# Optimization experiments

Measured on AMD Instinct MI355X. Metric: run time of the kernel, lower is better.

Reference implementation:

```python
import jax, jax.numpy as jnp
import numpy as np

L, B, S, D, H, F = 4, 2, 2048, 768, 12, 3072
HD = D // H
EPS = 1e-5


def _ln(x, g, b):
    m = jnp.mean(x, axis=-1, keepdims=True)
    v = jnp.mean((x - m) ** 2, axis=-1, keepdims=True)
    return (x - m) * jax.lax.rsqrt(v + EPS) * g + b


def setup_inputs() -> dict:
    key = jax.random.key(0)
    ks = jax.random.split(key, 12)
    s = 0.02
    n = lambda k, shp: jax.random.normal(k, shp, jnp.float32) * s
    return {
        "inputs": jax.random.normal(ks[0], (B, S, D), jnp.float32),
        "attn_mask": jax.random.randint(ks[1], (B, S, S), 0, 2) == 1,
        "Wq": n(ks[2], (L, D, D)), "bq": jnp.zeros((L, D), jnp.float32),
        "Wk": n(ks[3], (L, D, D)), "bk": jnp.zeros((L, D), jnp.float32),
        "Wv": n(ks[4], (L, D, D)), "bv": jnp.zeros((L, D), jnp.float32),
        "Wo": n(ks[5], (L, D, D)), "bo": jnp.zeros((L, D), jnp.float32),
        "ln1_g": jnp.ones((L, D), jnp.float32), "ln1_b": jnp.zeros((L, D), jnp.float32),
        "W1": n(ks[6], (L, F, D)), "b1": jnp.zeros((L, F), jnp.float32),
        "W2": n(ks[7], (L, D, F)), "b2": jnp.zeros((L, D), jnp.float32),
        "ln2_g": jnp.ones((L, D), jnp.float32), "ln2_b": jnp.zeros((L, D), jnp.float32),
    }


def reference(inputs, attn_mask, Wq, bq, Wk, bk, Wv, bv, Wo, bo,
              ln1_g, ln1_b, W1, b1, W2, b2, ln2_g, ln2_b):
    x = inputs
    scale = 1.0 / (HD ** 0.5)
    mask = attn_mask[:, None, :, :]  # [B,1,S,S] broadcasts over heads
    nlayers = Wq.shape[0]
    for i in range(nlayers):
        # torch Linear: y = x @ W.T + b, W stored [out,in]
        q = (jnp.einsum('bsd,ed->bse', x, Wq[i]) + bq[i]).reshape(B, S, H, HD)
        k = (jnp.einsum('bsd,ed->bse', x, Wk[i]) + bk[i]).reshape(B, S, H, HD)
        v = (jnp.einsum('bsd,ed->bse', x, Wv[i]) + bv[i]).reshape(B, S, H, HD)
        scores = jnp.einsum('bqhd,bkhd->bhqk', q, k) * scale
        scores = jnp.where(mask, jnp.float32(-1e9), scores)
        p = jax.nn.softmax(scores, axis=-1)
        ctx = jnp.einsum('bhqk,bkhd->bqhd', p, v).reshape(B, S, D)
        attn = jnp.einsum('bsd,ed->bse', ctx, Wo[i]) + bo[i]
        x = _ln(attn + x, ln1_g[i], ln1_b[i])
        h = jax.nn.relu(jnp.einsum('bsd,fd->bsf', x, W1[i]) + b1[i])
        ff = jnp.einsum('bsf,df->bsd', h, W2[i]) + b2[i]
        x = _ln(ff + x, ln2_g[i], ln2_b[i])
    return x
```

## Files before the change

kernel.cpp:

```cpp
#include <hip/hip_runtime.h>
#include <cmath>
#include <cstdint>
#include <cstddef>


typedef __bf16 bf16_t;
typedef __bf16 bf16x8 __attribute__((ext_vector_type(8)));
typedef __bf16 bf16x4 __attribute__((ext_vector_type(4)));
typedef float  f32x4  __attribute__((ext_vector_type(4)));
typedef float  f32x16 __attribute__((ext_vector_type(16)));
typedef int    i32x2  __attribute__((ext_vector_type(2)));

#define DEV static __device__ __forceinline__

constexpr int Lc = 4, Bc = 2, Sc = 2048, Dc = 768, Hc = 12, Fc = 3072, HDc = 64;
constexpr int Mrows = Bc * Sc;
#define QSCALE 0.18033688011112042f

DEV f32x4 mfma16(bf16x8 a, bf16x8 b, f32x4 c) {
  return __builtin_amdgcn_mfma_f32_16x16x32_bf16(a, b, c, 0, 0, 0);
}
DEV f32x16 mfma32(bf16x8 a, bf16x8 b, f32x16 c) {
  return __builtin_amdgcn_mfma_f32_32x32x16_bf16(a, b, c, 0, 0, 0);
}

DEV void gload_lds16(const void* g, void* l) {
  __builtin_amdgcn_global_load_lds(
      (const __attribute__((address_space(1))) void*)g,
      (__attribute__((address_space(3))) void*)l,
      16, 0, 0);
}

DEV float fexp2(float x) { return __builtin_amdgcn_exp2f(x); }

DEV unsigned cvtpk(float lo, float hi_) {
  unsigned r;
  asm("v_cvt_pk_bf16_f32 %0, %1, %2" : "=v"(r) : "v"(lo), "v"(hi_));
  return r;
}
DEV void swapl(unsigned &a, unsigned &b) {
  i32x2 r = __builtin_amdgcn_permlane32_swap((int)a, (int)b, false, false);
  a = (unsigned)r[0];
  b = (unsigned)r[1];
}
DEV bf16x8 frag4(unsigned a, unsigned b, unsigned c, unsigned d) {
  union { unsigned u[4]; bf16x8 v; } x;
  x.u[0] = a; x.u[1] = b; x.u[2] = c; x.u[3] = d;
  return x.v;
}


__global__ __launch_bounds__(256) void cvt_bf16_kernel(const float* __restrict__ in,
                                                       bf16_t* __restrict__ out, int n) {
  int i = (blockIdx.x * 256 + threadIdx.x) * 4;
  if (i + 3 < n) {
    float4 v = *(const float4*)(in + i);
    bf16x4 o;
    o[0] = (bf16_t)v.x; o[1] = (bf16_t)v.y; o[2] = (bf16_t)v.z; o[3] = (bf16_t)v.w;
    *(bf16x4*)(out + i) = o;
  }
}

__global__ __launch_bounds__(256) void cvt_qkv_kernel(const float* __restrict__ in,
                                                      bf16_t* __restrict__ out,
                                                      int which, int n) {
  int i = (blockIdx.x * 256 + threadIdx.x) * 4;
  if (i + 3 < n) {
    int l = i / (Dc * Dc);
    float4 v = *(const float4*)(in + i);
    bf16x4 o;
    o[0] = (bf16_t)v.x; o[1] = (bf16_t)v.y; o[2] = (bf16_t)v.z; o[3] = (bf16_t)v.w;
    *(bf16x4*)(out + (size_t)i + (size_t)(2 * l + which) * Dc * Dc) = o;
  }
}

__global__ __launch_bounds__(256) void init_x_kernel(const float* __restrict__ in,
                                                     float* __restrict__ x,
                                                     bf16_t* __restrict__ xb, int n) {
  int i = (blockIdx.x * 256 + threadIdx.x) * 4;
  if (i + 3 < n) {
    float4 v = *(const float4*)(in + i);
    *(float4*)(x + i) = v;
    bf16x4 o;
    o[0] = (bf16_t)v.x; o[1] = (bf16_t)v.y; o[2] = (bf16_t)v.z; o[3] = (bf16_t)v.w;
    *(bf16x4*)(xb + i) = o;
  }
}

__global__ __launch_bounds__(256) void mask_packT_kernel(const int* __restrict__ m,
                                                         unsigned long long* __restrict__ bits) {
  size_t gid = (size_t)blockIdx.x * 256 + threadIdx.x;
  int l = (int)(gid & 63);
  size_t widx = gid >> 6;
  size_t q = widx & (Sc - 1);
  size_t bkw = widx >> 11;
  size_t kw = bkw & (Sc / 64 - 1);
  size_t b = bkw >> 5;
  unsigned long long bm = __ballot(m[(b * Sc + q) * Sc + kw * 64 + l] != 0);
  if (l == 0) bits[widx] = bm;
}

template <int MF, int EPI>
__global__ __launch_bounds__(256) void gemm_bt(const bf16_t* __restrict__ A,
                                               const bf16_t* __restrict__ Bm,
                                               const float* __restrict__ bias,
                                               float* __restrict__ Cf,
                                               bf16_t* __restrict__ Cb,
                                               int M, int N, int K) {
  constexpr int BM = MF * 32;
  __shared__ bf16_t sA[BM * 64];
  __shared__ bf16_t sB[128 * 64];
  const int tid = threadIdx.x;
  const int w = tid >> 6, l = tid & 63, lg = l >> 4, li = l & 15;
  const int wr = w >> 1, wc = w & 1;
  const int tm = blockIdx.x * BM, tn = blockIdx.y * 128;

  f32x4 acc[MF][4];
#pragma unroll
  for (int m = 0; m < MF; m++)
#pragma unroll
    for (int n = 0; n < 4; n++) acc[m][n] = (f32x4){0.f, 0.f, 0.f, 0.f};

  for (int k0 = 0; k0 < K; k0 += 64) {
#pragma unroll
    for (int i = 0; i < MF; i++) {
      int off = i * 2048 + tid * 8;
      gload_lds16(A + (size_t)(tm + (off >> 6)) * K + k0 + (off & 63),
                  &sA[i * 2048 + w * 512]);
    }
#pragma unroll
    for (int i = 0; i < 4; i++) {
      int off = i * 2048 + tid * 8;
      gload_lds16(Bm + (size_t)(tn + (off >> 6)) * K + k0 + (off & 63),
                  &sB[i * 2048 + w * 512]);
    }
    __syncthreads();
#pragma unroll
    for (int kk = 0; kk < 2; kk++) {
      bf16x8 af[MF], bfr[4];
#pragma unroll
      for (int m = 0; m < MF; m++)
        af[m] = *(const bf16x8*)&sA[(wr * MF * 16 + m * 16 + li) * 64 + kk * 32 + lg * 8];
#pragma unroll
      for (int n = 0; n < 4; n++)
        bfr[n] = *(const bf16x8*)&sB[(wc * 64 + n * 16 + li) * 64 + kk * 32 + lg * 8];
#pragma unroll
      for (int m = 0; m < MF; m++)
#pragma unroll
        for (int n = 0; n < 4; n++)
          acc[m][n] = mfma16(af[m], bfr[n], acc[m][n]);
    }
    __syncthreads();
  }

#pragma unroll
  for (int m = 0; m < MF; m++) {
    int rbase = tm + wr * MF * 16 + m * 16 + lg * 4;
#pragma unroll
    for (int n = 0; n < 4; n++) {
      int c = tn + wc * 64 + n * 16 + li;
      float bv = bias[c];
#pragma unroll
      for (int j = 0; j < 4; j++) {
        float v = acc[m][n][j] + bv;
        size_t idx = (size_t)(rbase + j) * N + c;
        if constexpr (EPI == 0) Cf[idx] = v;
        else Cb[idx] = (bf16_t)fmaxf(v, 0.f);
      }
    }
  }
}

__global__ __launch_bounds__(256) void gemm_qkv(const bf16_t* __restrict__ A,
                                                const bf16_t* __restrict__ Bm,
                                                const float* __restrict__ bq,
                                                const float* __restrict__ bk,
                                                const float* __restrict__ bv,
                                                bf16_t* __restrict__ qo,
                                                bf16_t* __restrict__ ko,
                                                bf16_t* __restrict__ vTo) {
  constexpr int K = Dc;
  __shared__ bf16_t sA[64 * 64];
  __shared__ bf16_t sB[128 * 64];
  const int tid = threadIdx.x;
  const int w = tid >> 6, l = tid & 63, lg = l >> 4, li = l & 15;
  const int wr = w >> 1, wc = w & 1;
  const int tm = blockIdx.x * 64, tn = blockIdx.y * 128;

  f32x4 acc[2][4];
#pragma unroll
  for (int m = 0; m < 2; m++)
#pragma unroll
    for (int n = 0; n < 4; n++) acc[m][n] = (f32x4){0.f, 0.f, 0.f, 0.f};

  for (int k0 = 0; k0 < K; k0 += 64) {
#pragma unroll
    for (int i = 0; i < 2; i++) {
      int off = i * 2048 + tid * 8;
      gload_lds16(A + (size_t)(tm + (off >> 6)) * K + k0 + (off & 63),
                  &sA[i * 2048 + w * 512]);
    }
#pragma unroll
    for (int i = 0; i < 4; i++) {
      int off = i * 2048 + tid * 8;
      gload_lds16(Bm + (size_t)(tn + (off >> 6)) * K + k0 + (off & 63),
                  &sB[i * 2048 + w * 512]);
    }
    __syncthreads();
#pragma unroll
    for (int kk = 0; kk < 2; kk++) {
      bf16x8 af[2], bfr[4];
#pragma unroll
      for (int m = 0; m < 2; m++)
        af[m] = *(const bf16x8*)&sA[(wr * 32 + m * 16 + li) * 64 + kk * 32 + lg * 8];
#pragma unroll
      for (int n = 0; n < 4; n++)
        bfr[n] = *(const bf16x8*)&sB[(wc * 64 + n * 16 + li) * 64 + kk * 32 + lg * 8];
#pragma unroll
      for (int m = 0; m < 2; m++)
#pragma unroll
        for (int n = 0; n < 4; n++)
          acc[m][n] = mfma16(af[m], bfr[n], acc[m][n]);
    }
    __syncthreads();
  }

  const int which = tn / 768;
#pragma unroll
  for (int m = 0; m < 2; m++) {
    int rbase = tm + wr * 32 + m * 16 + lg * 4;
#pragma unroll
    for (int n = 0; n < 4; n++) {
      int c = tn + wc * 64 + n * 16 + li;
      int col = c - which * 768;
      if (which == 0) {
        float bvv = bq[col];
#pragma unroll
        for (int j = 0; j < 4; j++)
          qo[(size_t)(rbase + j) * Dc + col] = (bf16_t)((acc[m][n][j] + bvv) * QSCALE);
      } else if (which == 1) {
        float bvv = bk[col];
#pragma unroll
        for (int j = 0; j < 4; j++)
          ko[(size_t)(rbase + j) * Dc + col] = (bf16_t)(acc[m][n][j] + bvv);
      } else {
        float bvv = bv[col];
        int h = col >> 6, d = col & 63;
        int b = rbase >> 11, s0 = rbase & 2047;
        bf16x4 pk;
#pragma unroll
        for (int j = 0; j < 4; j++) pk[j] = (bf16_t)(acc[m][n][j] + bvv);
        *(bf16x4*)(vTo + ((size_t)(b * Hc + h) * HDc + d) * Sc + s0) = pk;
      }
    }
  }
}

__global__ __launch_bounds__(128) void attn3_kernel(
    const bf16_t* __restrict__ q, const bf16_t* __restrict__ k,
    const bf16_t* __restrict__ vT, const unsigned long long* __restrict__ maskT,
    bf16_t* __restrict__ ctx) {
  __shared__ __align__(16) char smem[32768];

  const int t = threadIdx.x, w = t >> 6, l = t & 63;
  const int hi = l >> 5, li = l & 31, lx = li & 7;
  const int gid = blockIdx.x;
  const int rest = gid >> 3;
  const int qt = rest & 31, bh = (gid & 7) + 8 * (rest >> 5);
  const int b = bh / Hc, h = bh - b * Hc;
  const int qbase = qt * 64;
  const int qrow = qbase + w * 32 + li;

  const bf16_t* qp = q + (size_t)(b * Sc + qrow) * Dc + h * HDc + hi * 8;
  bf16x8 qf[4];
#pragma unroll
  for (int dk = 0; dk < 4; dk++) qf[dk] = *(const bf16x8*)(qp + dk * 16);

  const bf16_t* kg = k + (size_t)(b * Sc) * Dc + h * HDc;
  const bf16_t* vg = vT + (size_t)bh * HDc * Sc;
  const unsigned long long* mg = maskT + (size_t)b * (Sc / 64) * Sc + qrow;

  f32x16 o0, o1;
#pragma unroll
  for (int r = 0; r < 16; r++) { o0[r] = 0.f; o1[r] = 0.f; }
  float ps = 0.f;

  auto stage = [&](int buf, int c) {
    const int kv0 = c * 64;
    bf16_t* sk = (bf16_t*)(smem + buf * 8192);
    bf16_t* sv = (bf16_t*)(smem + 16384 + buf * 8192);
#pragma unroll
    for (int i = 0; i < 4; i++) {
      int s = i * 128 + t;
      int row = s >> 3, ch = s & 7;
      gload_lds16(kg + (size_t)(kv0 + row) * Dc + ((ch ^ (row & 7)) * 8),
                  sk + (i * 128 + w * 64) * 8);
    }
#pragma unroll
    for (int i = 0; i < 4; i++) {
      int s = i * 128 + t;
      int row = s >> 3, ch = s & 7;
      gload_lds16(vg + (size_t)row * Sc + kv0 + ((ch ^ (row & 7)) * 8),
                  sv + (i * 128 + w * 64) * 8);
    }
  };

  stage(0, 0);
  __syncthreads();
  int cur = 0;
  constexpr int NT = Sc / 64;
  for (int c = 0; c < NT; c++) {
    if (c + 1 < NT) stage(cur ^ 1, c + 1);
    unsigned long long mw = mg[(size_t)c * Sc];
    unsigned ms0 = ((unsigned)mw) >> (hi * 4);
    unsigned ms1 = ((unsigned)(mw >> 32)) >> (hi * 4);

    f32x16 sc0, sc1;
#pragma unroll
    for (int r = 0; r < 16; r++) { sc0[r] = 0.f; sc1[r] = 0.f; }
    const bf16_t* kb = (const bf16_t*)(smem + cur * 8192);
#pragma unroll
    for (int dk = 0; dk < 4; dk++) {
      int ch = dk * 2 + hi;
      bf16x8 ka0 = *(const bf16x8*)(kb + li * 64 + ((ch ^ lx) * 8));
      bf16x8 ka1 = *(const bf16x8*)(kb + (32 + li) * 64 + ((ch ^ lx) * 8));
      sc0 = mfma32(ka0, qf[dk], sc0);
      sc1 = mfma32(ka1, qf[dk], sc1);
    }

    unsigned pw[16];
#pragma unroll
    for (int r = 0; r < 16; r += 2) {
      int kbit = (r & 3) + 8 * (r >> 2);
      float a0 = fexp2(sc0[r]), a1 = fexp2(sc0[r + 1]);
      float b0 = fexp2(sc1[r]), b1 = fexp2(sc1[r + 1]);
      a0 = ((ms0 >> kbit) & 1u) ? 0.f : a0;
      a1 = ((ms0 >> (kbit + 1)) & 1u) ? 0.f : a1;
      b0 = ((ms1 >> kbit) & 1u) ? 0.f : b0;
      b1 = ((ms1 >> (kbit + 1)) & 1u) ? 0.f : b1;
      ps += (a0 + a1) + (b0 + b1);
      pw[r >> 1] = cvtpk(a0, a1);
      pw[8 + (r >> 1)] = cvtpk(b0, b1);
    }
    swapl(pw[0], pw[2]);  swapl(pw[1], pw[3]);
    swapl(pw[4], pw[6]);  swapl(pw[5], pw[7]);
    swapl(pw[8], pw[10]); swapl(pw[9], pw[11]);
    swapl(pw[12], pw[14]); swapl(pw[13], pw[15]);
    bf16x8 pb0 = frag4(pw[0], pw[1], pw[2], pw[3]);
    bf16x8 pb1 = frag4(pw[4], pw[5], pw[6], pw[7]);
    bf16x8 pb2 = frag4(pw[8], pw[9], pw[10], pw[11]);
    bf16x8 pb3 = frag4(pw[12], pw[13], pw[14], pw[15]);

    const bf16_t* vb = (const bf16_t*)(smem + 16384 + cur * 8192);
#pragma unroll
    for (int g = 0; g < 4; g++) {
      int ch = g * 2 + hi;
      bf16x8 va0 = *(const bf16x8*)(vb + li * 64 + ((ch ^ lx) * 8));
      bf16x8 va1 = *(const bf16x8*)(vb + (32 + li) * 64 + ((ch ^ lx) * 8));
      bf16x8 pbg = (g == 0) ? pb0 : (g == 1) ? pb1 : (g == 2) ? pb2 : pb3;
      o0 = mfma32(va0, pbg, o0);
      o1 = mfma32(va1, pbg, o1);
    }
    __syncthreads();
    cur ^= 1;
  }

  float tot = ps + __shfl_xor(ps, 32, 64);
  float inv = 1.f / tot;

  __syncthreads();
  char* so = smem + w * 4096;
#pragma unroll
  for (int g = 0; g < 4; g++) {
    unsigned u0 = cvtpk(o0[g * 4 + 0] * inv, o0[g * 4 + 1] * inv);
    unsigned u1 = cvtpk(o0[g * 4 + 2] * inv, o0[g * 4 + 3] * inv);
    unsigned v0 = cvtpk(o1[g * 4 + 0] * inv, o1[g * 4 + 1] * inv);
    unsigned v1 = cvtpk(o1[g * 4 + 2] * inv, o1[g * 4 + 3] * inv);
    *(uint2*)(so + li * 128 + ((g ^ lx) * 16) + hi * 8) = make_uint2(u0, u1);
    *(uint2*)(so + li * 128 + (((g + 4) ^ lx) * 16) + hi * 8) = make_uint2(v0, v1);
  }
  __syncthreads();
  bf16_t* cbase = ctx + (size_t)(b * Sc + qbase + w * 32) * Dc + h * HDc;
#pragma unroll
  for (int i = 0; i < 4; i++) {
    int s = i * 64 + l;
    int row = s >> 3, ch = s & 7;
    bf16x8 vv = *(const bf16x8*)(so + row * 128 + ((ch ^ (row & 7)) * 16));
    *(bf16x8*)(cbase + (size_t)row * Dc + ch * 8) = vv;
  }
}

__global__ __launch_bounds__(256) void ln_res_kernel(const float* __restrict__ a,
                                                     const float* r,
                                                     const float* __restrict__ g,
                                                     const float* __restrict__ bb,
                                                     float* xo, bf16_t* __restrict__ xb) {
  const int row = blockIdx.x;
  const int t = threadIdx.x;
  const float* pa = a + (size_t)row * Dc;
  const float* pr = r + (size_t)row * Dc;
  float v0 = pa[t] + pr[t];
  float v1 = pa[t + 256] + pr[t + 256];
  float v2 = pa[t + 512] + pr[t + 512];
  float s = v0 + v1 + v2;
  float sq = v0 * v0 + v1 * v1 + v2 * v2;
#pragma unroll
  for (int ofs = 1; ofs < 64; ofs <<= 1) {
    s += __shfl_xor(s, ofs, 64);
    sq += __shfl_xor(sq, ofs, 64);
  }
  __shared__ float red[8];
  const int w = t >> 6, l = t & 63;
  if (l == 0) { red[w] = s; red[4 + w] = sq; }
  __syncthreads();
  s = red[0] + red[1] + red[2] + red[3];
  sq = red[4] + red[5] + red[6] + red[7];
  const float mean = s * (1.f / Dc);
  const float var = sq * (1.f / Dc) - mean * mean;
  const float rs = rsqrtf(var + 1e-5f);
  float* po = xo + (size_t)row * Dc;
  bf16_t* pb = xb + (size_t)row * Dc;
#pragma unroll
  for (int i = 0; i < 3; i++) {
    int d = t + i * 256;
    float vv = (i == 0 ? v0 : (i == 1 ? v1 : v2));
    float ov = (vv - mean) * rs * g[d] + bb[d];
    po[d] = ov;
    pb[d] = (bf16_t)ov;
  }
}


extern "C" void kernel_launch(void* const* d_in, const int* in_sizes, int n_in,
                              void* d_out, int out_size, void* d_ws, size_t ws_size,
                              hipStream_t stream) {
  const float* inputs = (const float*)d_in[0];
  const int* amask = (const int*)d_in[1];
  const float* Wq = (const float*)d_in[2];
  const float* bq = (const float*)d_in[3];
  const float* Wk = (const float*)d_in[4];
  const float* bk = (const float*)d_in[5];
  const float* Wv = (const float*)d_in[6];
  const float* bv = (const float*)d_in[7];
  const float* Wo = (const float*)d_in[8];
  const float* bo = (const float*)d_in[9];
  const float* ln1_g = (const float*)d_in[10];
  const float* ln1_b = (const float*)d_in[11];
  const float* W1 = (const float*)d_in[12];
  const float* b1 = (const float*)d_in[13];
  const float* W2 = (const float*)d_in[14];
  const float* b2 = (const float*)d_in[15];
  const float* ln2_g = (const float*)d_in[16];
  const float* ln2_b = (const float*)d_in[17];
  float* xout = (float*)d_out;

  char* p = (char*)d_ws;
  auto carve = [&](size_t bytes) -> char* {
    char* r = p;
    p += (bytes + 255) & ~(size_t)255;
    return r;
  };
  const size_t nDD = (size_t)Lc * Dc * Dc;
  const size_t nFD = (size_t)Lc * Fc * Dc;
  const size_t nAct = (size_t)Mrows * Dc;
  const size_t nHid = (size_t)Mrows * Fc;

  bf16_t* wqkv16 = (bf16_t*)carve(nDD * 3 * 2);
  bf16_t* wo16 = (bf16_t*)carve(nDD * 2);
  bf16_t* w1_16 = (bf16_t*)carve(nFD * 2);
  bf16_t* w2_16 = (bf16_t*)carve(nFD * 2);
  bf16_t* xb = (bf16_t*)carve(nAct * 2);
  bf16_t* q16 = (bf16_t*)carve(nAct * 2);
  bf16_t* k16 = (bf16_t*)carve(nAct * 2);
  bf16_t* vTb = (bf16_t*)carve(nAct * 2);
  bf16_t* ctx = (bf16_t*)carve(nAct * 2);
  bf16_t* h16 = (bf16_t*)carve(nHid * 2);
  float* attnf = (float*)carve(nAct * 4);
  float* ff = (float*)carve(nAct * 4);
  unsigned long long* maskb = (unsigned long long*)carve((size_t)Bc * (Sc / 64) * Sc * 8);
  (void)ws_size; (void)n_in; (void)in_sizes; (void)out_size;

  dim3 blk(256);

  mask_packT_kernel<<<(int)((size_t)Bc * Sc * Sc / 256), blk, 0, stream>>>(amask, maskb);
  cvt_qkv_kernel<<<(int)(nDD / 1024), blk, 0, stream>>>(Wq, wqkv16, 0, (int)nDD);
  cvt_qkv_kernel<<<(int)(nDD / 1024), blk, 0, stream>>>(Wk, wqkv16, 1, (int)nDD);
  cvt_qkv_kernel<<<(int)(nDD / 1024), blk, 0, stream>>>(Wv, wqkv16, 2, (int)nDD);
  cvt_bf16_kernel<<<(int)(nDD / 1024), blk, 0, stream>>>(Wo, wo16, (int)nDD);
  cvt_bf16_kernel<<<(int)(nFD / 1024), blk, 0, stream>>>(W1, w1_16, (int)nFD);
  cvt_bf16_kernel<<<(int)(nFD / 1024), blk, 0, stream>>>(W2, w2_16, (int)nFD);
  init_x_kernel<<<(int)(nAct / 1024), blk, 0, stream>>>(inputs, xout, xb, (int)nAct);

  for (int i = 0; i < Lc; i++) {
    const bf16_t* wqkv_l = wqkv16 + (size_t)i * 3 * Dc * Dc;
    const bf16_t* wo_l = wo16 + (size_t)i * Dc * Dc;
    const bf16_t* w1_l = w1_16 + (size_t)i * Fc * Dc;
    const bf16_t* w2_l = w2_16 + (size_t)i * Dc * Fc;

    gemm_qkv<<<dim3(Mrows / 64, 18), blk, 0, stream>>>(
        xb, wqkv_l, bq + (size_t)i * Dc, bk + (size_t)i * Dc, bv + (size_t)i * Dc,
        q16, k16, vTb);

    attn3_kernel<<<768, dim3(128), 0, stream>>>(q16, k16, vTb, maskb, ctx);

    gemm_bt<2, 0><<<dim3(Mrows / 64, Dc / 128), blk, 0, stream>>>(
        ctx, wo_l, bo + (size_t)i * Dc, attnf, nullptr, Mrows, Dc, Dc);
    ln_res_kernel<<<Mrows, blk, 0, stream>>>(attnf, xout, ln1_g + (size_t)i * Dc,
                                             ln1_b + (size_t)i * Dc, xout, xb);
    gemm_bt<4, 2><<<dim3(Mrows / 128, Fc / 128), blk, 0, stream>>>(
        xb, w1_l, b1 + (size_t)i * Fc, nullptr, h16, Mrows, Fc, Dc);
    gemm_bt<2, 0><<<dim3(Mrows / 64, Dc / 128), blk, 0, stream>>>(
        h16, w2_l, b2 + (size_t)i * Dc, ff, nullptr, Mrows, Dc, Fc);
    ln_res_kernel<<<Mrows, blk, 0, stream>>>(ff, xout, ln2_g + (size_t)i * Dc,
                                             ln2_b + (size_t)i * Dc, xout, xb);
  }
}
```

Baseline: 920.7 us.

## Split attention KV range across wave pairs and enlarge QKV/FFN2 GEMM tiles

```diff
diff --git a/kernel.cpp b/kernel.cpp
--- a/kernel.cpp
+++ b/kernel.cpp
@@ -180,22 +180,22 @@
                                                 bf16_t* __restrict__ ko,
                                                 bf16_t* __restrict__ vTo) {
   constexpr int K = Dc;
-  __shared__ bf16_t sA[64 * 64];
+  __shared__ bf16_t sA[128 * 64];
   __shared__ bf16_t sB[128 * 64];
   const int tid = threadIdx.x;
   const int w = tid >> 6, l = tid & 63, lg = l >> 4, li = l & 15;
   const int wr = w >> 1, wc = w & 1;
-  const int tm = blockIdx.x * 64, tn = blockIdx.y * 128;
-
-  f32x4 acc[2][4];
-#pragma unroll
-  for (int m = 0; m < 2; m++)
+  const int tm = blockIdx.x * 128, tn = blockIdx.y * 128;
+
+  f32x4 acc[4][4];
+#pragma unroll
+  for (int m = 0; m < 4; m++)
 #pragma unroll
     for (int n = 0; n < 4; n++) acc[m][n] = (f32x4){0.f, 0.f, 0.f, 0.f};
 
   for (int k0 = 0; k0 < K; k0 += 64) {
 #pragma unroll
-    for (int i = 0; i < 2; i++) {
+    for (int i = 0; i < 4; i++) {
       int off = i * 2048 + tid * 8;
       gload_lds16(A + (size_t)(tm + (off >> 6)) * K + k0 + (off & 63),
                   &sA[i * 2048 + w * 512]);
@@ -209,15 +209,15 @@
     __syncthreads();
 #pragma unroll
     for (int kk = 0; kk < 2; kk++) {
-      bf16x8 af[2], bfr[4];
-#pragma unroll
-      for (int m = 0; m < 2; m++)
-        af[m] = *(const bf16x8*)&sA[(wr * 32 + m * 16 + li) * 64 + kk * 32 + lg * 8];
+      bf16x8 af[4], bfr[4];
+#pragma unroll
+      for (int m = 0; m < 4; m++)
+        af[m] = *(const bf16x8*)&sA[(wr * 64 + m * 16 + li) * 64 + kk * 32 + lg * 8];
 #pragma unroll
       for (int n = 0; n < 4; n++)
         bfr[n] = *(const bf16x8*)&sB[(wc * 64 + n * 16 + li) * 64 + kk * 32 + lg * 8];
 #pragma unroll
-      for (int m = 0; m < 2; m++)
+      for (int m = 0; m < 4; m++)
 #pragma unroll
         for (int n = 0; n < 4; n++)
           acc[m][n] = mfma16(af[m], bfr[n], acc[m][n]);
@@ -227,8 +227,8 @@
 
   const int which = tn / 768;
 #pragma unroll
-  for (int m = 0; m < 2; m++) {
-    int rbase = tm + wr * 32 + m * 16 + lg * 4;
+  for (int m = 0; m < 4; m++) {
+    int rbase = tm + wr * 64 + m * 16 + lg * 4;
 #pragma unroll
     for (int n = 0; n < 4; n++) {
       int c = tn + wc * 64 + n * 16 + li;
@@ -256,61 +256,40 @@
   }
 }
 
-__global__ __launch_bounds__(128) void attn3_kernel(
+__global__ __launch_bounds__(256) void attn4_kernel(
     const bf16_t* __restrict__ q, const bf16_t* __restrict__ k,
     const bf16_t* __restrict__ vT, const unsigned long long* __restrict__ maskT,
     bf16_t* __restrict__ ctx) {
-  __shared__ __align__(16) char smem[32768];
+  __shared__ __align__(16) char smem[16896];
 
   const int t = threadIdx.x, w = t >> 6, l = t & 63;
   const int hi = l >> 5, li = l & 31, lx = li & 7;
+  const int wp = w & 1, kvh = w >> 1;
   const int gid = blockIdx.x;
   const int rest = gid >> 3;
   const int qt = rest & 31, bh = (gid & 7) + 8 * (rest >> 5);
   const int b = bh / Hc, h = bh - b * Hc;
   const int qbase = qt * 64;
-  const int qrow = qbase + w * 32 + li;
+  const int qrow = qbase + wp * 32 + li;
 
   const bf16_t* qp = q + (size_t)(b * Sc + qrow) * Dc + h * HDc + hi * 8;
   bf16x8 qf[4];
 #pragma unroll
   for (int dk = 0; dk < 4; dk++) qf[dk] = *(const bf16x8*)(qp + dk * 16);
 
-  const bf16_t* kg = k + (size_t)(b * Sc) * Dc + h * HDc;
-  const bf16_t* vg = vT + (size_t)bh * HDc * Sc;
-  const unsigned long long* mg = maskT + (size_t)b * (Sc / 64) * Sc + qrow;
+  const bf16_t* kg = k + ((size_t)(b * Sc) + kvh * 1024) * Dc + h * HDc;
+  const bf16_t* vg = vT + (size_t)bh * HDc * Sc + kvh * 1024;
+  const unsigned long long* mg =
+      maskT + (size_t)b * (Sc / 64) * Sc + (size_t)(kvh * 16) * Sc + qrow;
 
   f32x16 o0, o1;
 #pragma unroll
   for (int r = 0; r < 16; r++) { o0[r] = 0.f; o1[r] = 0.f; }
   float ps = 0.f;
 
-  auto stage = [&](int buf, int c) {
-    const int kv0 = c * 64;
-    bf16_t* sk = (bf16_t*)(smem + buf * 8192);
-    bf16_t* sv = (bf16_t*)(smem + 16384 + buf * 8192);
-#pragma unroll
-    for (int i = 0; i < 4; i++) {
-      int s = i * 128 + t;
-      int row = s >> 3, ch = s & 7;
-      gload_lds16(kg + (size_t)(kv0 + row) * Dc + ((ch ^ (row & 7)) * 8),
-                  sk + (i * 128 + w * 64) * 8);
-    }
-#pragma unroll
-    for (int i = 0; i < 4; i++) {
-      int s = i * 128 + t;
-      int row = s >> 3, ch = s & 7;
-      gload_lds16(vg + (size_t)row * Sc + kv0 + ((ch ^ (row & 7)) * 8),
-                  sv + (i * 128 + w * 64) * 8);
-    }
-  };
-
-  stage(0, 0);
-  __syncthreads();
-  int cur = 0;
-  constexpr int NT = Sc / 64;
-  for (int c = 0; c < NT; c++) {
-    if (c + 1 < NT) stage(cur ^ 1, c + 1);
+  for (int c = 0; c < 16; c++) {
+    const bf16_t* kp = kg + (size_t)(c * 64) * Dc;
+    const bf16_t* vp = vg + c * 64;
     unsigned long long mw = mg[(size_t)c * Sc];
     unsigned ms0 = ((unsigned)mw) >> (hi * 4);
     unsigned ms1 = ((unsigned)(mw >> 32)) >> (hi * 4);
@@ -318,12 +297,11 @@
     f32x16 sc0, sc1;
 #pragma unroll
     for (int r = 0; r < 16; r++) { sc0[r] = 0.f; sc1[r] = 0.f; }
-    const bf16_t* kb = (const bf16_t*)(smem + cur * 8192);
 #pragma unroll
     for (int dk = 0; dk < 4; dk++) {
       int ch = dk * 2 + hi;
-      bf16x8 ka0 = *(const bf16x8*)(kb + li * 64 + ((ch ^ lx) * 8));
-      bf16x8 ka1 = *(const bf16x8*)(kb + (32 + li) * 64 + ((ch ^ lx) * 8));
+      bf16x8 ka0 = *(const bf16x8*)(kp + (size_t)li * Dc + ch * 8);
+      bf16x8 ka1 = *(const bf16x8*)(kp + (size_t)(32 + li) * Dc + ch * 8);
       sc0 = mfma32(ka0, qf[dk], sc0);
       sc1 = mfma32(ka1, qf[dk], sc1);
     }
@@ -351,42 +329,67 @@
     bf16x8 pb2 = frag4(pw[8], pw[9], pw[10], pw[11]);
     bf16x8 pb3 = frag4(pw[12], pw[13], pw[14], pw[15]);
 
-    const bf16_t* vb = (const bf16_t*)(smem + 16384 + cur * 8192);
 #pragma unroll
     for (int g = 0; g < 4; g++) {
       int ch = g * 2 + hi;
-      bf16x8 va0 = *(const bf16x8*)(vb + li * 64 + ((ch ^ lx) * 8));
-      bf16x8 va1 = *(const bf16x8*)(vb + (32 + li) * 64 + ((ch ^ lx) * 8));
+      bf16x8 va0 = *(const bf16x8*)(vp + (size_t)li * Sc + ch * 8);
+      bf16x8 va1 = *(const bf16x8*)(vp + (size_t)(32 + li) * Sc + ch * 8);
       bf16x8 pbg = (g == 0) ? pb0 : (g == 1) ? pb1 : (g == 2) ? pb2 : pb3;
       o0 = mfma32(va0, pbg, o0);
       o1 = mfma32(va1, pbg, o1);
     }
-    __syncthreads();
-    cur ^= 1;
-  }
-
-  float tot = ps + __shfl_xor(ps, 32, 64);
-  float inv = 1.f / tot;
-
+  }
+
+  float* mp = (float*)(smem + 16384);
+  {
+    char* base = smem + wp * 8192 + l * 128;
+    if (kvh == 1) {
+#pragma unroll
+      for (int r = 0; r < 4; r++) {
+        *(f32x4*)(base + ((r ^ (l & 7)) * 16)) =
+            (f32x4){o0[r * 4], o0[r * 4 + 1], o0[r * 4 + 2], o0[r * 4 + 3]};
+        *(f32x4*)(base + (((r + 4) ^ (l & 7)) * 16)) =
+            (f32x4){o1[r * 4], o1[r * 4 + 1], o1[r * 4 + 2], o1[r * 4 + 3]};
+      }
+      mp[wp * 64 + l] = ps;
+    }
+  }
   __syncthreads();
-  char* so = smem + w * 4096;
-#pragma unroll
-  for (int g = 0; g < 4; g++) {
-    unsigned u0 = cvtpk(o0[g * 4 + 0] * inv, o0[g * 4 + 1] * inv);
-    unsigned u1 = cvtpk(o0[g * 4 + 2] * inv, o0[g * 4 + 3] * inv);
-    unsigned v0 = cvtpk(o1[g * 4 + 0] * inv, o1[g * 4 + 1] * inv);
-    unsigned v1 = cvtpk(o1[g * 4 + 2] * inv, o1[g * 4 + 3] * inv);
-    *(uint2*)(so + li * 128 + ((g ^ lx) * 16) + hi * 8) = make_uint2(u0, u1);
-    *(uint2*)(so + li * 128 + (((g + 4) ^ lx) * 16) + hi * 8) = make_uint2(v0, v1);
+  float inv = 0.f;
+  if (kvh == 0) {
+    char* base = smem + wp * 8192 + l * 128;
+#pragma unroll
+    for (int r = 0; r < 4; r++) {
+      f32x4 u = *(const f32x4*)(base + ((r ^ (l & 7)) * 16));
+      f32x4 v = *(const f32x4*)(base + (((r + 4) ^ (l & 7)) * 16));
+#pragma unroll
+      for (int j = 0; j < 4; j++) { o0[r * 4 + j] += u[j]; o1[r * 4 + j] += v[j]; }
+    }
+    ps += mp[wp * 64 + l];
+    float tot = ps + __shfl_xor(ps, 32, 64);
+    inv = 1.f / tot;
   }
   __syncthreads();
-  bf16_t* cbase = ctx + (size_t)(b * Sc + qbase + w * 32) * Dc + h * HDc;
-#pragma unroll
-  for (int i = 0; i < 4; i++) {
-    int s = i * 64 + l;
-    int row = s >> 3, ch = s & 7;
-    bf16x8 vv = *(const bf16x8*)(so + row * 128 + ((ch ^ (row & 7)) * 16));
-    *(bf16x8*)(cbase + (size_t)row * Dc + ch * 8) = vv;
+  if (kvh == 0) {
+    char* so = smem + wp * 4096;
+#pragma unroll
+    for (int g = 0; g < 4; g++) {
+      unsigned u0 = cvtpk(o0[g * 4 + 0] * inv, o0[g * 4 + 1] * inv);
+      unsigned u1 = cvtpk(o0[g * 4 + 2] * inv, o0[g * 4 + 3] * inv);
+      unsigned v0 = cvtpk(o1[g * 4 + 0] * inv, o1[g * 4 + 1] * inv);
+      unsigned v1 = cvtpk(o1[g * 4 + 2] * inv, o1[g * 4 + 3] * inv);
+      *(uint2*)(so + li * 128 + ((g ^ lx) * 16) + hi * 8) = make_uint2(u0, u1);
+      *(uint2*)(so + li * 128 + (((g + 4) ^ lx) * 16) + hi * 8) = make_uint2(v0, v1);
+    }
+    __builtin_amdgcn_s_waitcnt(0);
+    bf16_t* cbase = ctx + (size_t)(b * Sc + qbase + wp * 32) * Dc + h * HDc;
+#pragma unroll
+    for (int i = 0; i < 4; i++) {
+      int s = i * 64 + l;
+      int row = s >> 3, ch = s & 7;
+      bf16x8 vv = *(const bf16x8*)(so + row * 128 + ((ch ^ (row & 7)) * 16));
+      *(bf16x8*)(cbase + (size_t)row * Dc + ch * 8) = vv;
+    }
   }
 }
 
@@ -497,11 +500,11 @@
     const bf16_t* w1_l = w1_16 + (size_t)i * Fc * Dc;
     const bf16_t* w2_l = w2_16 + (size_t)i * Dc * Fc;
 
-    gemm_qkv<<<dim3(Mrows / 64, 18), blk, 0, stream>>>(
+    gemm_qkv<<<dim3(Mrows / 128, 18), blk, 0, stream>>>(
         xb, wqkv_l, bq + (size_t)i * Dc, bk + (size_t)i * Dc, bv + (size_t)i * Dc,
         q16, k16, vTb);
 
-    attn3_kernel<<<768, dim3(128), 0, stream>>>(q16, k16, vTb, maskb, ctx);
+    attn4_kernel<<<768, blk, 0, stream>>>(q16, k16, vTb, maskb, ctx);
 
     gemm_bt<2, 0><<<dim3(Mrows / 64, Dc / 128), blk, 0, stream>>>(
         ctx, wo_l, bo + (size_t)i * Dc, attnf, nullptr, Mrows, Dc, Dc);
@@ -509,7 +512,7 @@
                                              ln1_b + (size_t)i * Dc, xout, xb);
     gemm_bt<4, 2><<<dim3(Mrows / 128, Fc / 128), blk, 0, stream>>>(
         xb, w1_l, b1 + (size_t)i * Fc, nullptr, h16, Mrows, Fc, Dc);
-    gemm_bt<2, 0><<<dim3(Mrows / 64, Dc / 128), blk, 0, stream>>>(
+    gemm_bt<4, 0><<<dim3(Mrows / 128, Dc / 128), blk, 0, stream>>>(
         h16, w2_l, b2 + (size_t)i * Dc, ff, nullptr, Mrows, Dc, Fc);
     ln_res_kernel<<<Mrows, blk, 0, stream>>>(ff, xout, ln2_g + (size_t)i * Dc,
                                              ln2_b + (size_t)i * Dc, xout, xb);
```

Result: slower. 1.153 ms (+25.3%).
